# Optimization experiments

Measured on AMD Instinct MI355X. Metric: run time of the kernel, lower is better.

Reference implementation:

```python
import jax, jax.numpy as jnp
import numpy as np
from jax import lax

# ---- configuration (matches init_kwargs) ----
B, C_DATA, C_FEAT, H, W = 2, 8, 8, 160, 160
K = 7                      # number of soft nearest neighbors
PS, STRIDE, WIN = 10, 5, 15
FEAT, C_EMB = 64, 8
N1 = (H - PS) // STRIDE + 1   # 31, no padding needed
N2 = (W - PS) // STRIDE + 1   # 31
NEG_INF = -1e9


def _conv3(x, w, b):
    y = lax.conv_general_dilated(x, w, (1, 1), 'SAME',
                                 dimension_numbers=('NCHW', 'OIHW', 'NCHW'))
    return y + b[None, :, None, None]


def _cnn(x, w1, b1, w2, b2, w3, b3):
    # depth-3 DnCNN-style net: conv-relu-conv-relu-conv (bn=False, lastact=linear)
    h = jax.nn.relu(_conv3(x, w1, b1))
    h = jax.nn.relu(_conv3(h, w2, b2))
    return _conv3(h, w3, b3)


def _im2patch(x):
    # x: [b,c,H,W] -> [b,n1,n2,c*PS*PS]; patch flattened channel-major (c,p1,p2)
    ii = jnp.arange(N1)[:, None] * STRIDE + jnp.arange(PS)[None, :]  # [n1,PS]
    jj = jnp.arange(N2)[:, None] * STRIDE + jnp.arange(PS)[None, :]  # [n2,PS]
    p = x[:, :, ii[:, None, :, None], jj[None, :, None, :]]  # [b,c,n1,n2,PS,PS]
    p = jnp.transpose(p, (0, 2, 3, 1, 4, 5))
    return p.reshape(p.shape[0], N1, N2, -1)


def _n3block(x_data, x_faet, ew1, eb1, ew2, eb2, ew3, eb3,
             tw1, tb1, tw2, tb2, tw3, tb3):
    xe = _cnn(x_faet, ew1, eb1, ew2, eb2, ew3, eb3)      # [b,8,H,W] embeddings
    log_temp = _cnn(x_faet, tw1, tb1, tw2, tb2, tw3, tb3)  # [b,1,H,W]

    ye = _im2patch(xe)                        # [b,n1,n2,E]; queries == database
    yp = _im2patch(x_data)                    # [b,n1,n2,F]
    lt = _im2patch(log_temp).mean(-1)         # scalar log-temp per patch
    temp = jnp.exp(lt)[..., None]             # [b,n1,n2,1] (temp_bias = 1)

    S = min(WIN, N1, N2)
    R = S // 2
    base1 = jnp.clip(jnp.arange(N1) - R, 0, N1 - S)   # clamped window top-left
    base2 = jnp.clip(jnp.arange(N2) - R, 0, N2 - S)
    offs = jnp.stack(jnp.meshgrid(jnp.arange(S), jnp.arange(S), indexing='ij'),
                     axis=-1).reshape(-1, 2)          # [S*S,2]
    i1, i2 = jnp.arange(N1), jnp.arange(N2)
    yn = jnp.sum(ye * ye, axis=-1)            # [b,n1,n2] squared norms

    @jax.checkpoint
    def dist_step(carry, off):
        j1 = base1 + off[0]
        j2 = base2 + off[1]
        xs = ye[:, j1][:, :, j2]              # [b,n1,n2,E] candidate embedding
        xn = yn[:, j1][:, :, j2]
        dot = jnp.einsum('bije,bije->bij', ye, xs)
        d = yn + xn - 2.0 * dot               # squared euclidean distance
        self_m = (j1 == i1)[:, None] & (j2 == i2)[None, :]
        return carry, (d, self_m)

    _, (D, selfm) = lax.scan(dist_step, None, offs)
    D = jnp.moveaxis(D, 0, -1)                # [b,n1,n2,O], O=S*S
    selfm = jnp.moveaxis(selfm, 0, -1)        # [n1,n2,O]

    logits = -D / temp
    logits = jnp.where(selfm, NEG_INF, logits)   # exclude_self

    # continuous deterministic top-k (N3Net): w_j = softmax(a); a += log(1 - w_j)
    ws = []
    for _ in range(K):
        wgt = jax.nn.softmax(logits, axis=-1)
        ws.append(wgt)
        logits = logits + jnp.log1p(-jnp.minimum(wgt, 1.0 - 1e-6))
    Wk = jnp.stack(ws, axis=-1)               # [b,n1,n2,O,K]

    @jax.checkpoint
    def agg_step(z, args):
        off, wk = args                        # wk: [b,n1,n2,K]
        j1 = base1 + off[0]
        j2 = base2 + off[1]
        ys = yp[:, j1][:, :, j2]              # [b,n1,n2,F]
        return z + wk[..., :, None] * ys[..., None, :], None

    z0 = jnp.zeros(yp.shape[:3] + (K, yp.shape[-1]), yp.dtype)
    z, _ = lax.scan(agg_step, z0, (offs, jnp.moveaxis(Wk, 3, 0)))
    z = z - yp[..., None, :]                  # residue=True
    out_p = jnp.concatenate([yp[..., None, :], z], axis=3)  # [b,n1,n2,K+1,F]

    # fold patch volumes back to image, averaging overlaps
    b = out_p.shape[0]
    C = (K + 1) * C_DATA
    out_p = out_p.reshape(b, N1, N2, K + 1, C_DATA, PS, PS)
    out_p = jnp.transpose(out_p, (0, 3, 4, 1, 2, 5, 6)).reshape(b, C, N1, N2, PS, PS)
    rows = jnp.arange(N1)[:, None] * STRIDE + jnp.arange(PS)[None, :]
    cols = jnp.arange(N2)[:, None] * STRIDE + jnp.arange(PS)[None, :]
    lin = (rows[:, None, :, None] * W + cols[None, :, None, :]).reshape(-1)
    vals = out_p.reshape(b, C, -1)
    img = jnp.zeros((b, C, H * W), out_p.dtype).at[:, :, lin].add(vals)
    cnt = jnp.zeros((H * W,), out_p.dtype).at[lin].add(1.0)
    return (img / cnt).reshape(b, C, H, W)


def setup_inputs() -> dict:
    key = jax.random.key(0)
    ks = jax.random.split(key, 8)
    f32 = jnp.float32
    wn = lambda k, s: jax.random.normal(k, s, f32) * 0.05
    return dict(
        x_data=jax.random.normal(ks[0], (B, C_DATA, H, W), f32),
        x_faet=jax.random.normal(ks[1], (B, C_FEAT, H, W), f32),
        ew1=wn(ks[2], (FEAT, C_FEAT, 3, 3)), eb1=jnp.zeros((FEAT,), f32),
        ew2=wn(ks[3], (FEAT, FEAT, 3, 3)), eb2=jnp.zeros((FEAT,), f32),
        ew3=wn(ks[4], (C_EMB, FEAT, 3, 3)), eb3=jnp.zeros((C_EMB,), f32),
        tw1=wn(ks[5], (FEAT, C_FEAT, 3, 3)), tb1=jnp.zeros((FEAT,), f32),
        tw2=wn(ks[6], (FEAT, FEAT, 3, 3)), tb2=jnp.zeros((FEAT,), f32),
        tw3=wn(ks[7], (1, FEAT, 3, 3)), tb3=jnp.zeros((1,), f32),
    )


def reference(x_data, x_faet, ew1, eb1, ew2, eb2, ew3, eb3,
              tw1, tb1, tw2, tb2, tw3, tb3):
    return _n3block(x_data, x_faet, ew1, eb1, ew2, eb2, ew3, eb3,
                    tw1, tb1, tw2, tb2, tw3, tb3)
```

## Files before the change

kernel.cpp:

```cpp
#include <hip/hip_runtime.h>
#include <math.h>

#define BN 2
#define HH 160
#define WW 160
#define CDATA 8
#define PS 10
#define STR 5
#define N1 31
#define N2 31
#define NSITE (N1*N2)
#define SITES (BN*NSITE)
#define SWIN 15
#define NOFF 225
#define KK 7
#define EDIM 800
#define NPIX 25600
#define LP 40
#define KP 480
#define COLP 992
#define GP 34
#define KSPLIT 5

typedef __attribute__((ext_vector_type(8))) short s8v;
typedef __attribute__((ext_vector_type(8))) unsigned short u8v;
typedef __attribute__((ext_vector_type(4))) float f4v;

__device__ __forceinline__ unsigned short f2bf(float f) {
    unsigned u = __float_as_uint(f);
    return (unsigned short)((u + 0x7FFFu + ((u >> 16) & 1u)) >> 16);
}
__device__ __forceinline__ float bf2f(unsigned short h) {
    return __uint_as_float(((unsigned)h) << 16);
}

__device__ __forceinline__ float block_sum(float v, float* sred) {
    #pragma unroll
    for (int o = 32; o; o >>= 1) v += __shfl_xor(v, o);
    __syncthreads();
    if ((threadIdx.x & 63) == 0) sred[threadIdx.x >> 6] = v;
    __syncthreads();
    return sred[0] + sred[1] + sred[2] + sred[3];
}

__global__ __launch_bounds__(256) void prep_k(const float* __restrict__ xd,
                                              const float* __restrict__ ew2,
                                              const float* __restrict__ tw2,
                                              const float* __restrict__ ew1,
                                              const float* __restrict__ tw1,
                                              const float* __restrict__ ew3,
                                              const float* __restrict__ tw3,
                                              unsigned short* __restrict__ ypT,
                                              unsigned short* __restrict__ wp,
                                              unsigned short* __restrict__ wp1,
                                              unsigned short* __restrict__ wp3) {
    int blk = blockIdx.x;
    int t = threadIdx.x;
    if (blk < 1600) {
        int b = blk / 800, e = blk % 800;
        int cd = e & 7, pp = e >> 3;
        int pi = pp / 10, pj = pp % 10;
        const float* src = xd + ((size_t)(b * 8 + cd) * HH + pi) * WW + pj;
        unsigned short* dst = ypT + (size_t)blk * COLP;
        for (int it = 0; it < 4; ++it) {
            int col = it * 256 + t;
            if (col < COLP) {
                int j1 = col >> 5, j2 = col & 31;
                unsigned short v = 0;
                if (j2 < 31) v = f2bf(src[(j1 * 5) * WW + j2 * 5]);
                dst[col] = v;
            }
        }
    } else if (blk < 1888) {
        int idx = (blk - 1600) * 256 + t;
        int which = idx / (64 * 576); int r = idx % (64 * 576);
        int n = r / 576, k = r % 576;
        int p = k / 64, c = k % 64;
        const float* w = which ? tw2 : ew2;
        wp[idx] = f2bf(w[(n * 64 + c) * 9 + p]);
    } else if (blk < 1936) {
        int idx = (blk - 1888) * 256 + t;
        if (idx < 128 * 96) {
            int n = idx / 96, k = idx % 96;
            int tap = k >> 3, c = k & 7;
            unsigned short v = 0;
            if (tap < 9) {
                const float* w = (n < 64) ? ew1 : tw1;
                v = f2bf(w[((n & 63) * 8 + c) * 9 + tap]);
            }
            wp1[idx] = v;
        }
    } else {
        int idx = (blk - 1936) * 256 + t;
        if (idx < 2 * 16 * 576) {
            int which = idx / (16 * 576); int r = idx % (16 * 576);
            int n = r / 576, k = r % 576;
            int tap = k / 64, c = k % 64;
            float w = 0.f; bool lo = false;
            if (which == 0) { w = ew3[((n & 7) * 64 + c) * 9 + tap]; lo = (n >= 8); }
            else if (n < 2) { w = tw3[c * 9 + tap]; lo = (n == 1); }
            unsigned short hi = f2bf(w);
            wp3[idx] = lo ? f2bf(w - bf2f(hi)) : hi;
            if (which == 1 && n >= 2) wp3[idx] = 0;
        }
    }
}

__global__ __launch_bounds__(256) void conv1_mfma_k(const float* __restrict__ xf,
                                                    const unsigned short* __restrict__ wp1,
                                                    const float* __restrict__ eb1,
                                                    const float* __restrict__ tb1,
                                                    unsigned short* __restrict__ h1) {
    __shared__ unsigned short Al[128 * LP];
    __shared__ unsigned short Bl[64 * LP];
    const int t = threadIdx.x;
    const int m0 = blockIdx.x * 64;
    const int wv = t >> 6, lane = t & 63;
    f4v acc[2][4];
    #pragma unroll
    for (int fj = 0; fj < 2; ++fj)
        #pragma unroll
        for (int fi = 0; fi < 4; ++fi) { f4v z = {0.f,0.f,0.f,0.f}; acc[fj][fi] = z; }
    const int mp = m0 + (t >> 2);
    const int b = mp / NPIX, rp = mp % NPIX;
    const int py = rp / WW, px = rp % WW;
    for (int ks = 0; ks < 3; ++ks) {
        int tap = ks * 4 + (t & 3);
        int dy = tap / 3 - 1, dx = tap % 3 - 1;
        int yy = py + dy, xx = px + dx;
        bool ok = (tap < 9) && yy >= 0 && yy < HH && xx >= 0 && xx < WW;
        u8v bv;
        #pragma unroll
        for (int c = 0; c < 8; ++c)
            bv[c] = ok ? f2bf(xf[((size_t)(b * 8 + c)) * NPIX + yy * WW + xx]) : 0;
        __syncthreads();
        *(u8v*)(Bl + (t >> 2) * LP + (t & 3) * 8) = bv;
        #pragma unroll
        for (int it = 0; it < 2; ++it) {
            int idx = t + it * 256;
            int row = idx >> 2, seg = idx & 3;
            *(u8v*)(Al + row * LP + seg * 8) = *(const u8v*)(wp1 + row * 96 + ks * 32 + seg * 8);
        }
        __syncthreads();
        s8v af[2], bf[4];
        #pragma unroll
        for (int fj = 0; fj < 2; ++fj)
            af[fj] = *(const s8v*)((const short*)Al + (wv * 32 + fj * 16 + (lane & 15)) * LP + (lane >> 4) * 8);
        #pragma unroll
        for (int fi = 0; fi < 4; ++fi)
            bf[fi] = *(const s8v*)((const short*)Bl + (fi * 16 + (lane & 15)) * LP + (lane >> 4) * 8);
        #pragma unroll
        for (int fj = 0; fj < 2; ++fj)
            #pragma unroll
            for (int fi = 0; fi < 4; ++fi)
                acc[fj][fi] = __builtin_amdgcn_mfma_f32_16x16x32_bf16(af[fj], bf[fi], acc[fj][fi], 0, 0, 0);
    }
    #pragma unroll
    for (int fj = 0; fj < 2; ++fj) {
        int nb = wv * 32 + fj * 16 + (lane >> 4) * 4;
        float bias4[4];
        #pragma unroll
        for (int c = 0; c < 4; ++c) {
            int n = nb + c;
            bias4[c] = (n < 64) ? eb1[n] : tb1[n - 64];
        }
        #pragma unroll
        for (int fi = 0; fi < 4; ++fi) {
            int mm = m0 + fi * 16 + (lane & 15);
            ushort4 o;
            o.x = f2bf(fmaxf(acc[fj][fi][0] + bias4[0], 0.f));
            o.y = f2bf(fmaxf(acc[fj][fi][1] + bias4[1], 0.f));
            o.z = f2bf(fmaxf(acc[fj][fi][2] + bias4[2], 0.f));
            o.w = f2bf(fmaxf(acc[fj][fi][3] + bias4[3], 0.f));
            *(ushort4*)(h1 + (size_t)mm * 128 + nb) = o;
        }
    }
}

__global__ __launch_bounds__(256) void conv2_mfma_k(const unsigned short* __restrict__ h1,
                                                    const unsigned short* __restrict__ wp,
                                                    const float* __restrict__ eb2,
                                                    const float* __restrict__ tb2,
                                                    unsigned short* __restrict__ h2) {
    __shared__ unsigned short Al[64 * LP];
    __shared__ unsigned short Bl[128 * LP];
    const int t = threadIdx.x;
    const int which = blockIdx.y;
    const int m0 = blockIdx.x * 128;
    const int wv = t >> 6, lane = t & 63;
    f4v acc[4][2];
    #pragma unroll
    for (int nf = 0; nf < 4; ++nf)
        #pragma unroll
        for (int mf = 0; mf < 2; ++mf) { f4v z = {0.f,0.f,0.f,0.f}; acc[nf][mf] = z; }
    const unsigned short* wb = wp + (size_t)which * 64 * 576;
    const int sm = t >> 2, sq = (t & 3) * 8;
    const int mp0 = m0 + sm;
    const int b0 = mp0 / NPIX, rp0 = mp0 % NPIX;
    const int py0 = rp0 / WW, px0 = rp0 % WW;
    const int mp1 = m0 + 64 + sm;
    const int b1_ = mp1 / NPIX, rp1 = mp1 % NPIX;
    const int py1 = rp1 / WW, px1 = rp1 % WW;
    for (int step = 0; step < 18; ++step) {
        const int p = step >> 1, ch = (step & 1) * 32;
        const int dy = p / 3 - 1, dx = p % 3 - 1;
        s8v av = *(const s8v*)(wb + sm * 576 + p * 64 + ch + sq);
        s8v bv0, bv1;
        #pragma unroll
        for (int j = 0; j < 8; j++) { bv0[j] = 0; bv1[j] = 0; }
        int yy = py0 + dy, xx = px0 + dx;
        if (yy >= 0 && yy < HH && xx >= 0 && xx < WW)
            bv0 = *(const s8v*)((const short*)h1 + ((size_t)b0 * NPIX + yy * WW + xx) * 128 + which * 64 + ch + sq);
        yy = py1 + dy; xx = px1 + dx;
        if (yy >= 0 && yy < HH && xx >= 0 && xx < WW)
            bv1 = *(const s8v*)((const short*)h1 + ((size_t)b1_ * NPIX + yy * WW + xx) * 128 + which * 64 + ch + sq);
        __syncthreads();
        *(s8v*)((short*)Al + sm * LP + sq) = av;
        *(s8v*)((short*)Bl + sm * LP + sq) = bv0;
        *(s8v*)((short*)Bl + (64 + sm) * LP + sq) = bv1;
        __syncthreads();
        s8v af[4], bf[2];
        #pragma unroll
        for (int nf = 0; nf < 4; ++nf)
            af[nf] = *(const s8v*)((const short*)Al + (nf * 16 + (lane & 15)) * LP + (lane >> 4) * 8);
        #pragma unroll
        for (int mf = 0; mf < 2; ++mf)
            bf[mf] = *(const s8v*)((const short*)Bl + (wv * 32 + mf * 16 + (lane & 15)) * LP + (lane >> 4) * 8);
        #pragma unroll
        for (int nf = 0; nf < 4; ++nf)
            #pragma unroll
            for (int mf = 0; mf < 2; ++mf)
                acc[nf][mf] = __builtin_amdgcn_mfma_f32_16x16x32_bf16(af[nf], bf[mf], acc[nf][mf], 0, 0, 0);
    }
    const float* bias = which ? tb2 : eb2;
    #pragma unroll
    for (int nf = 0; nf < 4; ++nf) {
        int nb = nf * 16 + (lane >> 4) * 4;
        f4v bv4 = *(const f4v*)(bias + nb);
        #pragma unroll
        for (int mf = 0; mf < 2; ++mf) {
            int mm = m0 + wv * 32 + mf * 16 + (lane & 15);
            ushort4 o;
            o.x = f2bf(fmaxf(acc[nf][mf][0] + bv4[0], 0.f));
            o.y = f2bf(fmaxf(acc[nf][mf][1] + bv4[1], 0.f));
            o.z = f2bf(fmaxf(acc[nf][mf][2] + bv4[2], 0.f));
            o.w = f2bf(fmaxf(acc[nf][mf][3] + bv4[3], 0.f));
            *(ushort4*)(h2 + ((size_t)which * 51200 + mm) * 64 + nb) = o;
        }
    }
}

__global__ __launch_bounds__(256) void conv3_mfma_k(const unsigned short* __restrict__ h2,
                                                    const unsigned short* __restrict__ wp3,
                                                    const float* __restrict__ eb3,
                                                    const float* __restrict__ tb3,
                                                    float* __restrict__ xe,
                                                    float* __restrict__ ltm) {
    __shared__ unsigned short Al[16 * LP];
    __shared__ unsigned short Bl[128 * LP];
    const int t = threadIdx.x;
    const int which = blockIdx.y;
    const int m0 = blockIdx.x * 128;
    const int wv = t >> 6, lane = t & 63;
    f4v acc[2];
    { f4v z = {0.f,0.f,0.f,0.f}; acc[0] = z; acc[1] = z; }
    const unsigned short* wb = wp3 + (size_t)which * 16 * 576;
    const int sm = t >> 2, sq = (t & 3) * 8;
    const int mp0 = m0 + sm;
    const int b0 = mp0 / NPIX, rp0 = mp0 % NPIX;
    const int py0 = rp0 / WW, px0 = rp0 % WW;
    const int mp1 = m0 + 64 + sm;
    const int b1_ = mp1 / NPIX, rp1 = mp1 % NPIX;
    const int py1 = rp1 / WW, px1 = rp1 % WW;
    for (int step = 0; step < 18; ++step) {
        const int p = step >> 1, ch = (step & 1) * 32;
        const int dy = p / 3 - 1, dx = p % 3 - 1;
        s8v av;
        if (t < 64) av = *(const s8v*)(wb + (t >> 2) * 576 + p * 64 + ch + (t & 3) * 8);
        s8v bv0, bv1;
        #pragma unroll
        for (int j = 0; j < 8; j++) { bv0[j] = 0; bv1[j] = 0; }
        int yy = py0 + dy, xx = px0 + dx;
        if (yy >= 0 && yy < HH && xx >= 0 && xx < WW)
            bv0 = *(const s8v*)((const short*)h2 + ((size_t)which * 51200 + (size_t)b0 * NPIX + yy * WW + xx) * 64 + ch + sq);
        yy = py1 + dy; xx = px1 + dx;
        if (yy >= 0 && yy < HH && xx >= 0 && xx < WW)
            bv1 = *(const s8v*)((const short*)h2 + ((size_t)which * 51200 + (size_t)b1_ * NPIX + yy * WW + xx) * 64 + ch + sq);
        __syncthreads();
        if (t < 64) *(s8v*)((short*)Al + (t >> 2) * LP + (t & 3) * 8) = av;
        *(s8v*)((short*)Bl + sm * LP + sq) = bv0;
        *(s8v*)((short*)Bl + (64 + sm) * LP + sq) = bv1;
        __syncthreads();
        s8v af = *(const s8v*)((const short*)Al + (lane & 15) * LP + (lane >> 4) * 8);
        #pragma unroll
        for (int mf = 0; mf < 2; ++mf) {
            s8v bf = *(const s8v*)((const short*)Bl + (wv * 32 + mf * 16 + (lane & 15)) * LP + (lane >> 4) * 8);
            acc[mf] = __builtin_amdgcn_mfma_f32_16x16x32_bf16(af, bf, acc[mf], 0, 0, 0);
        }
    }
    #pragma unroll
    for (int mf = 0; mf < 2; ++mf) {
        int mm = m0 + wv * 32 + mf * 16 + (lane & 15);
        if (which == 0) {
            f4v hilo;
            #pragma unroll
            for (int c = 0; c < 4; ++c)
                hilo[c] = acc[mf][c] + __shfl_xor(acc[mf][c], 32);
            if (lane < 32) {
                int nb = (lane >> 4) * 4;
                f4v o;
                #pragma unroll
                for (int c = 0; c < 4; ++c) o[c] = hilo[c] + eb3[nb + c];
                *(f4v*)(xe + (size_t)mm * 8 + nb) = o;
            }
        } else {
            if ((lane >> 4) == 0)
                ltm[mm] = acc[mf][0] + acc[mf][1] + tb3[0];
        }
    }
}

__global__ __launch_bounds__(256) void im2patch_k(const float* __restrict__ xe,
                                                  const float* __restrict__ ltm,
                                                  unsigned short* __restrict__ yeH,
                                                  unsigned short* __restrict__ yeL,
                                                  float* __restrict__ yn,
                                                  float* __restrict__ tempv) {
    __shared__ float sred[4];
    int site = blockIdx.x;
    int b = site / NSITE; int ij = site % NSITE;
    int i1 = ij / N2, i2 = ij % N2;
    int t = threadIdx.x;
    const float* xeb = xe + (size_t)b * NPIX * 8;
    float ssq = 0.f;
    for (int e = t; e < EDIM; e += 256) {
        int rr = e / 80, rem = e % 80;
        float v = xeb[((size_t)(i1 * STR + rr) * WW + i2 * STR) * 8 + rem];
        unsigned short h = f2bf(v);
        float lo = v - bf2f(h);
        yeH[(size_t)site * EDIM + e] = h;
        yeL[(size_t)site * EDIM + e] = f2bf(lo);
        ssq += v * v;
    }
    float tot = block_sum(ssq, sred);
    if (t == 0) yn[site] = tot;
    float sl = 0.f;
    if (t < 100) {
        int rr = t / 10, q = t % 10;
        sl = ltm[(size_t)b * NPIX + (i1 * STR + rr) * WW + (i2 * STR + q)];
    }
    float slt = block_sum(sl, sred);
    if (t == 0) tempv[site] = expf(slt * (1.f / 100.f));
}

__global__ __launch_bounds__(256) void gram_mfma_k(const unsigned short* __restrict__ yeH,
                                                   const unsigned short* __restrict__ yeL,
                                                   float* __restrict__ dotsC) {
    __shared__ unsigned short AsH[32 * GP], AsL[32 * GP];
    __shared__ unsigned short BsH[256 * GP], BsL[256 * GP];
    int blk = blockIdx.x;
    int kc = blk % KSPLIT; int r = blk / KSPLIT;
    int nh = r & 1; r >>= 1;
    int b = r / N1, i1 = r % N1;
    int b1 = min(max(i1 - 7, 0), 16);
    int t = threadIdx.x;
    int wv = t >> 6, lane = t & 63;
    f4v acc[2][4];
    #pragma unroll
    for (int mt = 0; mt < 2; ++mt)
        #pragma unroll
        for (int nt = 0; nt < 4; ++nt) { f4v z = {0.f,0.f,0.f,0.f}; acc[mt][nt] = z; }
    const size_t abase = (size_t)((b * N1 + i1) * N2) * EDIM;
    for (int ks = kc * 5; ks < kc * 5 + 5; ++ks) {
        __syncthreads();
        {
            int idx = t & 127;
            int row = idx >> 2, seg = idx & 3;
            u8v v;
            #pragma unroll
            for (int u = 0; u < 8; ++u) v[u] = 0;
            if (row < 31)
                v = *(const u8v*)((t < 128 ? yeH : yeL) + abase + (size_t)row * EDIM + ks * 32 + seg * 8);
            *(u8v*)((t < 128 ? AsH : AsL) + row * GP + seg * 8) = v;
        }
        #pragma unroll
        for (int rep = 0; rep < 8; ++rep) {
            int idx = t + rep * 256;
            int isH = idx < 1024;
            int id2 = idx & 1023;
            int row = id2 >> 2, seg = id2 & 3;
            int dj = nh * 8 + (row >> 5), j2 = row & 31;
            u8v v;
            #pragma unroll
            for (int u = 0; u < 8; ++u) v[u] = 0;
            if (dj < 15 && j2 < 31) {
                size_t site = (size_t)((b * N1 + b1 + dj) * N2 + j2);
                v = *(const u8v*)((isH ? yeH : yeL) + site * EDIM + ks * 32 + seg * 8);
            }
            *(u8v*)((isH ? BsH : BsL) + row * GP + seg * 8) = v;
        }
        __syncthreads();
        s8v afH[2], afL[2], bfH[4], bfL[4];
        #pragma unroll
        for (int mt = 0; mt < 2; ++mt) {
            int ar = mt * 16 + (lane & 15);
            afH[mt] = *(const s8v*)((const short*)AsH + ar * GP + (lane >> 4) * 8);
            afL[mt] = *(const s8v*)((const short*)AsL + ar * GP + (lane >> 4) * 8);
        }
        #pragma unroll
        for (int nt = 0; nt < 4; ++nt) {
            int br = wv * 64 + nt * 16 + (lane & 15);
            bfH[nt] = *(const s8v*)((const short*)BsH + br * GP + (lane >> 4) * 8);
            bfL[nt] = *(const s8v*)((const short*)BsL + br * GP + (lane >> 4) * 8);
        }
        #pragma unroll
        for (int mt = 0; mt < 2; ++mt)
            #pragma unroll
            for (int nt = 0; nt < 4; ++nt) {
                acc[mt][nt] = __builtin_amdgcn_mfma_f32_16x16x32_bf16(afH[mt], bfH[nt], acc[mt][nt], 0, 0, 0);
                acc[mt][nt] = __builtin_amdgcn_mfma_f32_16x16x32_bf16(afH[mt], bfL[nt], acc[mt][nt], 0, 0, 0);
                acc[mt][nt] = __builtin_amdgcn_mfma_f32_16x16x32_bf16(afL[mt], bfH[nt], acc[mt][nt], 0, 0, 0);
            }
    }
    float* dk = dotsC + (size_t)kc * SITES * NOFF;
    #pragma unroll
    for (int mt = 0; mt < 2; ++mt) {
        int i2b = mt * 16 + (lane >> 4) * 4;
        #pragma unroll
        for (int nt = 0; nt < 4; ++nt) {
            int n = wv * 64 + nt * 16 + (lane & 15);
            int dj = nh * 8 + (n >> 5), j2 = n & 31;
            if (dj >= 15 || j2 >= 31) continue;
            #pragma unroll
            for (int c = 0; c < 4; ++c) {
                int i2 = i2b + c;
                if (i2 >= 31) continue;
                int b2 = min(max(i2 - 7, 0), 16);
                int dc = j2 - b2;
                if (dc < 0 || dc >= SWIN) continue;
                size_t site = (size_t)((b * N1 + i1) * N2 + i2);
                dk[site * NOFF + dj * SWIN + dc] = acc[mt][nt][c];
            }
        }
    }
}

__global__ __launch_bounds__(256) void softmax_awrite_k(const float* __restrict__ dotsC,
                                                        const float* __restrict__ yn,
                                                        const float* __restrict__ tempv,
                                                        unsigned short* __restrict__ Aglob) {
    __shared__ float sw[4][228];
    int wv = threadIdx.x >> 6, lane = threadIdx.x & 63;
    int wid = blockIdx.x * 4 + wv;
    bool active = (wid < SITES);
    int wids = active ? wid : (SITES - 1);
    int b = wids / NSITE; int ij = wids % NSITE;
    int i1 = ij / N2, i2 = ij % N2;
    int b1 = min(max(i1 - 7, 0), 16);
    int b2 = min(max(i2 - 7, 0), 16);
    int pglob = i2 >> 1, s = i2 & 1;
    unsigned short* Abase = Aglob + (size_t)((b * N1 + i1) * 256) * KP;
    float yns = yn[wids];
    float tvi = 1.f / tempv[wids];
    float lg[4];
    #pragma unroll
    for (int r = 0; r < 4; ++r) {
        int t = lane + 64 * r;
        lg[r] = -1e9f;
        if (t < NOFF) {
            float dot = 0.f;
            #pragma unroll
            for (int kc = 0; kc < KSPLIT; ++kc)
                dot += dotsC[((size_t)kc * SITES + wids) * NOFF + t];
            int dj = t / SWIN, dc = t % SWIN;
            int j1 = b1 + dj, j2 = b2 + dc;
            float xn = yn[(b * N1 + j1) * N2 + j2];
            float d = yns + xn - 2.f * dot;
            lg[r] = -d * tvi;
            if (j1 == i1 && j2 == i2) lg[r] = -1e9f;
        }
    }
    for (int k = 0; k < KK; ++k) {
        float m = fmaxf(fmaxf(lg[0], lg[1]), fmaxf(lg[2], lg[3]));
        #pragma unroll
        for (int o = 32; o; o >>= 1) m = fmaxf(m, __shfl_xor(m, o));
        float ex[4]; float ssum = 0.f;
        #pragma unroll
        for (int r = 0; r < 4; ++r) { ex[r] = __expf(lg[r] - m); ssum += ex[r]; }
        #pragma unroll
        for (int o = 32; o; o >>= 1) ssum += __shfl_xor(ssum, o);
        float inv = 1.f / ssum;
        #pragma unroll
        for (int r = 0; r < 4; ++r) {
            float wgt = ex[r] * inv;
            int t = lane + 64 * r;
            if (t < NOFF) sw[wv][t] = wgt;
            lg[r] += log1pf(-fminf(wgt, 1.f - 1e-6f));
        }
        __syncthreads();
        if (active && lane < 60) {
            u8v o;
            #pragma unroll
            for (int u = 0; u < 8; ++u) {
                int n = lane * 8 + u;
                int dj = n >> 5, j2 = n & 31;
                int dc = j2 - b2;
                o[u] = (j2 < 31 && dc >= 0 && dc < SWIN) ? f2bf(sw[wv][dj * SWIN + dc]) : (unsigned short)0;
            }
            int m_ = 16 * pglob + k + 7 * s;
            *(u8v*)(Abase + (size_t)m_ * KP + lane * 8) = o;
        }
        __syncthreads();
    }
    if (active && s == 0 && lane < 60) {
        u8v z;
        #pragma unroll
        for (int u = 0; u < 8; ++u) z[u] = 0;
        *(u8v*)(Abase + (size_t)(16 * pglob + 14) * KP + lane * 8) = z;
        *(u8v*)(Abase + (size_t)(16 * pglob + 15) * KP + lane * 8) = z;
        if (i2 == 30) {
            #pragma unroll
            for (int sl = 7; sl < 14; ++sl)
                *(u8v*)(Abase + (size_t)(16 * 15 + sl) * KP + lane * 8) = z;
        }
    }
}

__global__ __launch_bounds__(256) void agg_gemm_k(const unsigned short* __restrict__ Aglob,
                                                  const unsigned short* __restrict__ ypT,
                                                  unsigned short* __restrict__ zbuf) {
    __shared__ unsigned short As[128 * 40];
    __shared__ unsigned short Bs[160 * 40];
    int blk = blockIdx.x;
    int b = blk / 310; int r = blk % 310;
    int i1 = r / 10; int r2 = r % 10;
    int mh = r2 / 5, nc = r2 % 5;
    int b1 = min(max(i1 - 7, 0), 16);
    int t = threadIdx.x;
    int wv = t >> 6, lane = t & 63;
    int wm = (wv & 1) * 64, we = (wv >> 1) * 80;
    const unsigned short* Ab = Aglob + ((size_t)(b * N1 + i1) * 256 + mh * 128) * KP;
    const unsigned short* Bb = ypT + ((size_t)b * 800 + nc * 160) * COLP + b1 * 32;
    f4v accr[4][5];
    #pragma unroll
    for (int mt = 0; mt < 4; ++mt)
        #pragma unroll
        for (int et = 0; et < 5; ++et) { f4v z = {0.f,0.f,0.f,0.f}; accr[mt][et] = z; }
    for (int ks = 0; ks < 15; ++ks) {
        __syncthreads();
        #pragma unroll
        for (int it = 0; it < 2; ++it) {
            int idx = t + it * 256;
            int row = idx >> 2, seg = idx & 3;
            *(u8v*)(As + row * 40 + seg * 8) = *(const u8v*)(Ab + (size_t)row * KP + ks * 32 + seg * 8);
        }
        #pragma unroll
        for (int it = 0; it < 3; ++it) {
            int idx = t + it * 256;
            if (idx < 640) {
                int row = idx >> 2, seg = idx & 3;
                *(u8v*)(Bs + row * 40 + seg * 8) = *(const u8v*)(Bb + (size_t)row * COLP + ks * 32 + seg * 8);
            }
        }
        __syncthreads();
        s8v af[4], bf[5];
        #pragma unroll
        for (int mt = 0; mt < 4; ++mt)
            af[mt] = *(const s8v*)((const short*)As + (wm + mt * 16 + (lane & 15)) * 40 + (lane >> 4) * 8);
        #pragma unroll
        for (int et = 0; et < 5; ++et)
            bf[et] = *(const s8v*)((const short*)Bs + (we + et * 16 + (lane & 15)) * 40 + (lane >> 4) * 8);
        #pragma unroll
        for (int mt = 0; mt < 4; ++mt)
            #pragma unroll
            for (int et = 0; et < 5; ++et)
                accr[mt][et] = __builtin_amdgcn_mfma_f32_16x16x32_bf16(af[mt], bf[et], accr[mt][et], 0, 0, 0);
    }
    unsigned short* zb = zbuf + ((size_t)(b * N1 + i1) * 256 + mh * 128) * 800 + nc * 160;
    #pragma unroll
    for (int mt = 0; mt < 4; ++mt) {
        int mrow = wm + mt * 16 + (lane >> 4) * 4;
        #pragma unroll
        for (int et = 0; et < 5; ++et) {
            int ecol = we + et * 16 + (lane & 15);
            #pragma unroll
            for (int c = 0; c < 4; ++c)
                zb[(size_t)(mrow + c) * 800 + ecol] = f2bf(accr[mt][et][c]);
        }
    }
}

__global__ __launch_bounds__(256) void finalize_k(const unsigned short* __restrict__ zbuf,
                                                  const float* __restrict__ xd,
                                                  float* __restrict__ out) {
    int pid = blockIdx.x * 256 + threadIdx.x;
    if (pid >= BN * NPIX) return;
    int b = pid / NPIX, pix = pid % NPIX;
    int h = pix / WW, w_ = pix % WW;
    int lo1 = max(0, (h - 5) / 5),  hi1 = min(30, h / 5);
    int lo2 = max(0, (w_ - 5) / 5), hi2 = min(30, w_ / 5);
    float cntinv = 1.f / (float)((hi1 - lo1 + 1) * (hi2 - lo2 + 1));
    float xv[8];
    #pragma unroll
    for (int cd = 0; cd < 8; ++cd) {
        xv[cd] = xd[((size_t)(b * 8 + cd)) * NPIX + pix];
        out[((size_t)(b * 64 + cd)) * NPIX + pix] = xv[cd];
    }
    for (int k = 0; k < KK; ++k) {
        float s[8];
        #pragma unroll
        for (int cd = 0; cd < 8; ++cd) s[cd] = 0.f;
        for (int i1 = lo1; i1 <= hi1; ++i1) {
            int pi = h - 5 * i1;
            for (int i2 = lo2; i2 <= hi2; ++i2) {
                int pj = w_ - 5 * i2;
                int m = 16 * (i2 >> 1) + k + 7 * (i2 & 1);
                const unsigned short* zp = zbuf + ((size_t)(b * N1 + i1) * 256 + m) * 800 + (pi * 10 + pj) * 8;
                u8v zv = *(const u8v*)zp;
                #pragma unroll
                for (int cd = 0; cd < 8; ++cd) s[cd] += bf2f(zv[cd]);
            }
        }
        #pragma unroll
        for (int cd = 0; cd < 8; ++cd)
            out[((size_t)(b * 64 + (k + 1) * 8 + cd)) * NPIX + pix] = s[cd] * cntinv - xv[cd];
    }
}

extern "C" void kernel_launch(void* const* d_in, const int* in_sizes, int n_in,
                              void* d_out, int out_size, void* d_ws, size_t ws_size,
                              hipStream_t stream) {
    (void)in_sizes; (void)n_in; (void)out_size; (void)ws_size;
    const float* x_data = (const float*)d_in[0];
    const float* x_faet = (const float*)d_in[1];
    const float* ew1 = (const float*)d_in[2];  const float* eb1 = (const float*)d_in[3];
    const float* ew2 = (const float*)d_in[4];  const float* eb2 = (const float*)d_in[5];
    const float* ew3 = (const float*)d_in[6];  const float* eb3 = (const float*)d_in[7];
    const float* tw1 = (const float*)d_in[8];  const float* tb1 = (const float*)d_in[9];
    const float* tw2 = (const float*)d_in[10]; const float* tb2 = (const float*)d_in[11];
    const float* tw3 = (const float*)d_in[12]; const float* tb3 = (const float*)d_in[13];
    float* out = (float*)d_out;

    char* base = (char*)d_ws;
    unsigned short* h1 = (unsigned short*)(base);
    unsigned short* h2 = (unsigned short*)(base + 13107200);
    unsigned short* wp1 = (unsigned short*)(base + 13107200);
    unsigned short* wp = (unsigned short*)(base + 26214400);
    float* yn    = (float*)(base + 26361856);
    float* tempv = (float*)(base + 26370048);
    unsigned short* ypT = (unsigned short*)(base + 26378240);
    float* xe    = (float*)(base + 29552640);
    float* ltm   = (float*)(base + 31191040);
    unsigned short* yeH = (unsigned short*)(base + 31395840);
    unsigned short* yeL = (unsigned short*)(base + 34471040);
    unsigned short* wp3 = (unsigned short*)(base + 37546240);
    unsigned short* Aglob = (unsigned short*)(base + 29552640);
    float* dotsC = (float*)h2;
    unsigned short* zbuf = (unsigned short*)base;

    prep_k<<<2008, 256, 0, stream>>>(x_data, ew2, tw2, ew1, tw1, ew3, tw3, ypT, wp, wp1, wp3);
    conv1_mfma_k<<<800, 256, 0, stream>>>(x_faet, wp1, eb1, tb1, h1);
    conv2_mfma_k<<<dim3(400, 2), 256, 0, stream>>>(h1, wp, eb2, tb2, h2);
    conv3_mfma_k<<<dim3(400, 2), 256, 0, stream>>>(h2, wp3, eb3, tb3, xe, ltm);

    im2patch_k<<<BN * NSITE, 256, 0, stream>>>(xe, ltm, yeH, yeL, yn, tempv);
    gram_mfma_k<<<BN * N1 * 2 * KSPLIT, 256, 0, stream>>>(yeH, yeL, dotsC);
    softmax_awrite_k<<<(SITES + 3) / 4, 256, 0, stream>>>(dotsC, yn, tempv, Aglob);

    agg_gemm_k<<<BN * 310, 256, 0, stream>>>(Aglob, ypT, zbuf);
    finalize_k<<<(BN * NPIX + 255) / 256, 256, 0, stream>>>(zbuf, x_data, out);
}
```

Baseline: 170.7 us.

## Fuse bf16 hi/lo split into conv3 and gather patches directly in gram kernel

Conv3 now writes the embedding as bf16 hi/lo planes plus per-pixel squared sums, instead of fp32. The gram kernel reads patch elements straight from those pixel planes by computing im2patch addresses inline, so the materialized patch arrays (about 6 MB) are gone. A lighter per-site wave kernel sums the squared norms and log-temperatures. This removes the large im2patch write/read traffic and a kernel, at the cost of less contiguous gather loads in gram.

```diff
diff --git a/kernel.cpp b/kernel.cpp
--- a/kernel.cpp
+++ b/kernel.cpp
@@ -24,6 +24,7 @@
 
 typedef __attribute__((ext_vector_type(8))) short s8v;
 typedef __attribute__((ext_vector_type(8))) unsigned short u8v;
+typedef __attribute__((ext_vector_type(4))) unsigned short u4v;
 typedef __attribute__((ext_vector_type(4))) float f4v;
 
 __device__ __forceinline__ unsigned short f2bf(float f) {
@@ -32,15 +33,6 @@
 }
 __device__ __forceinline__ float bf2f(unsigned short h) {
     return __uint_as_float(((unsigned)h) << 16);
-}
-
-__device__ __forceinline__ float block_sum(float v, float* sred) {
-    #pragma unroll
-    for (int o = 32; o; o >>= 1) v += __shfl_xor(v, o);
-    __syncthreads();
-    if ((threadIdx.x & 63) == 0) sred[threadIdx.x >> 6] = v;
-    __syncthreads();
-    return sred[0] + sred[1] + sred[2] + sred[3];
 }
 
 __global__ __launch_bounds__(256) void prep_k(const float* __restrict__ xd,
@@ -254,7 +246,9 @@
                                                     const unsigned short* __restrict__ wp3,
                                                     const float* __restrict__ eb3,
                                                     const float* __restrict__ tb3,
-                                                    float* __restrict__ xe,
+                                                    unsigned short* __restrict__ xeH,
+                                                    unsigned short* __restrict__ xeL,
+                                                    float* __restrict__ splane,
                                                     float* __restrict__ ltm) {
     __shared__ unsigned short Al[16 * LP];
     __shared__ unsigned short Bl[128 * LP];
@@ -308,10 +302,20 @@
                 hilo[c] = acc[mf][c] + __shfl_xor(acc[mf][c], 32);
             if (lane < 32) {
                 int nb = (lane >> 4) * 4;
-                f4v o;
+                u4v hs, ls;
+                float ss = 0.f;
                 #pragma unroll
-                for (int c = 0; c < 4; ++c) o[c] = hilo[c] + eb3[nb + c];
-                *(f4v*)(xe + (size_t)mm * 8 + nb) = o;
+                for (int c = 0; c < 4; ++c) {
+                    float v = hilo[c] + eb3[nb + c];
+                    unsigned short h = f2bf(v);
+                    hs[c] = h;
+                    ls[c] = f2bf(v - bf2f(h));
+                    ss += v * v;
+                }
+                *(u4v*)(xeH + (size_t)mm * 8 + nb) = hs;
+                *(u4v*)(xeL + (size_t)mm * 8 + nb) = ls;
+                ss += __shfl_xor(ss, 16);
+                if (lane < 16) splane[mm] = ss;
             }
         } else {
             if ((lane >> 4) == 0)
@@ -320,41 +324,32 @@
     }
 }
 
-__global__ __launch_bounds__(256) void im2patch_k(const float* __restrict__ xe,
-                                                  const float* __restrict__ ltm,
-                                                  unsigned short* __restrict__ yeH,
-                                                  unsigned short* __restrict__ yeL,
-                                                  float* __restrict__ yn,
-                                                  float* __restrict__ tempv) {
-    __shared__ float sred[4];
-    int site = blockIdx.x;
-    int b = site / NSITE; int ij = site % NSITE;
+__global__ __launch_bounds__(256) void ynt_k(const float* __restrict__ splane,
+                                             const float* __restrict__ ltm,
+                                             float* __restrict__ yn,
+                                             float* __restrict__ tempv) {
+    int wv = threadIdx.x >> 6, lane = threadIdx.x & 63;
+    int wid = blockIdx.x * 4 + wv;
+    if (wid >= SITES) return;
+    int b = wid / NSITE; int ij = wid % NSITE;
     int i1 = ij / N2, i2 = ij % N2;
-    int t = threadIdx.x;
-    const float* xeb = xe + (size_t)b * NPIX * 8;
-    float ssq = 0.f;
-    for (int e = t; e < EDIM; e += 256) {
-        int rr = e / 80, rem = e % 80;
-        float v = xeb[((size_t)(i1 * STR + rr) * WW + i2 * STR) * 8 + rem];
-        unsigned short h = f2bf(v);
-        float lo = v - bf2f(h);
-        yeH[(size_t)site * EDIM + e] = h;
-        yeL[(size_t)site * EDIM + e] = f2bf(lo);
-        ssq += v * v;
-    }
-    float tot = block_sum(ssq, sred);
-    if (t == 0) yn[site] = tot;
-    float sl = 0.f;
-    if (t < 100) {
-        int rr = t / 10, q = t % 10;
-        sl = ltm[(size_t)b * NPIX + (i1 * STR + rr) * WW + (i2 * STR + q)];
-    }
-    float slt = block_sum(sl, sred);
-    if (t == 0) tempv[site] = expf(slt * (1.f / 100.f));
-}
-
-__global__ __launch_bounds__(256) void gram_mfma_k(const unsigned short* __restrict__ yeH,
-                                                   const unsigned short* __restrict__ yeL,
+    float s1 = 0.f, s2 = 0.f;
+    for (int p = lane; p < 100; p += 64) {
+        int rr = p / 10, q = p % 10;
+        int idx = b * NPIX + (i1 * STR + rr) * WW + i2 * STR + q;
+        s1 += splane[idx];
+        s2 += ltm[idx];
+    }
+    #pragma unroll
+    for (int o = 32; o; o >>= 1) { s1 += __shfl_xor(s1, o); s2 += __shfl_xor(s2, o); }
+    if (lane == 0) {
+        yn[wid] = s1;
+        tempv[wid] = expf(s2 * (1.f / 100.f));
+    }
+}
+
+__global__ __launch_bounds__(256) void gram_mfma_k(const unsigned short* __restrict__ xeH,
+                                                   const unsigned short* __restrict__ xeL,
                                                    float* __restrict__ dotsC) {
     __shared__ unsigned short AsH[32 * GP], AsL[32 * GP];
     __shared__ unsigned short BsH[256 * GP], BsL[256 * GP];
@@ -370,17 +365,21 @@
     for (int mt = 0; mt < 2; ++mt)
         #pragma unroll
         for (int nt = 0; nt < 4; ++nt) { f4v z = {0.f,0.f,0.f,0.f}; acc[mt][nt] = z; }
-    const size_t abase = (size_t)((b * N1 + i1) * N2) * EDIM;
+    const size_t pbase = (size_t)b * NPIX;
     for (int ks = kc * 5; ks < kc * 5 + 5; ++ks) {
         __syncthreads();
         {
             int idx = t & 127;
             int row = idx >> 2, seg = idx & 3;
+            int p = ks * 4 + seg;
+            int rr = p / 10, q = p - rr * 10;
             u8v v;
             #pragma unroll
             for (int u = 0; u < 8; ++u) v[u] = 0;
-            if (row < 31)
-                v = *(const u8v*)((t < 128 ? yeH : yeL) + abase + (size_t)row * EDIM + ks * 32 + seg * 8);
+            if (row < 31) {
+                size_t a = (pbase + (size_t)(i1 * STR + rr) * WW + row * STR + q) * 8;
+                v = *(const u8v*)((t < 128 ? xeH : xeL) + a);
+            }
             *(u8v*)((t < 128 ? AsH : AsL) + row * GP + seg * 8) = v;
         }
         #pragma unroll
@@ -390,12 +389,14 @@
             int id2 = idx & 1023;
             int row = id2 >> 2, seg = id2 & 3;
             int dj = nh * 8 + (row >> 5), j2 = row & 31;
+            int p = ks * 4 + seg;
+            int rr = p / 10, q = p - rr * 10;
             u8v v;
             #pragma unroll
             for (int u = 0; u < 8; ++u) v[u] = 0;
             if (dj < 15 && j2 < 31) {
-                size_t site = (size_t)((b * N1 + b1 + dj) * N2 + j2);
-                v = *(const u8v*)((isH ? yeH : yeL) + site * EDIM + ks * 32 + seg * 8);
+                size_t a = (pbase + (size_t)((b1 + dj) * STR + rr) * WW + j2 * STR + q) * 8;
+                v = *(const u8v*)((isH ? xeH : xeL) + a);
             }
             *(u8v*)((isH ? BsH : BsL) + row * GP + seg * 8) = v;
         }
@@ -649,10 +650,10 @@
     float* yn    = (float*)(base + 26361856);
     float* tempv = (float*)(base + 26370048);
     unsigned short* ypT = (unsigned short*)(base + 26378240);
-    float* xe    = (float*)(base + 29552640);
-    float* ltm   = (float*)(base + 31191040);
-    unsigned short* yeH = (unsigned short*)(base + 31395840);
-    unsigned short* yeL = (unsigned short*)(base + 34471040);
+    unsigned short* xeH = (unsigned short*)(base + 29552640);
+    unsigned short* xeL = (unsigned short*)(base + 30371840);
+    float* ltm    = (float*)(base + 31191040);
+    float* splane = (float*)(base + 31395840);
     unsigned short* wp3 = (unsigned short*)(base + 37546240);
     unsigned short* Aglob = (unsigned short*)(base + 29552640);
     float* dotsC = (float*)h2;
@@ -661,10 +662,10 @@
     prep_k<<<2008, 256, 0, stream>>>(x_data, ew2, tw2, ew1, tw1, ew3, tw3, ypT, wp, wp1, wp3);
     conv1_mfma_k<<<800, 256, 0, stream>>>(x_faet, wp1, eb1, tb1, h1);
     conv2_mfma_k<<<dim3(400, 2), 256, 0, stream>>>(h1, wp, eb2, tb2, h2);
-    conv3_mfma_k<<<dim3(400, 2), 256, 0, stream>>>(h2, wp3, eb3, tb3, xe, ltm);
-
-    im2patch_k<<<BN * NSITE, 256, 0, stream>>>(xe, ltm, yeH, yeL, yn, tempv);
-    gram_mfma_k<<<BN * N1 * 2 * KSPLIT, 256, 0, stream>>>(yeH, yeL, dotsC);
+    conv3_mfma_k<<<dim3(400, 2), 256, 0, stream>>>(h2, wp3, eb3, tb3, xeH, xeL, splane, ltm);
+
+    ynt_k<<<(SITES + 3) / 4, 256, 0, stream>>>(splane, ltm, yn, tempv);
+    gram_mfma_k<<<BN * N1 * 2 * KSPLIT, 256, 0, stream>>>(xeH, xeL, dotsC);
     softmax_awrite_k<<<(SITES + 3) / 4, 256, 0, stream>>>(dotsC, yn, tempv, Aglob);
 
     agg_gemm_k<<<BN * 310, 256, 0, stream>>>(Aglob, ypT, zbuf);
```

After: 165.0 us. 1.03x faster.
